# Kernel tuning notes

Measured on AMD Instinct MI355X. Metric: run time of the kernel, lower is better.

Reference implementation:

```python
import jax, jax.numpy as jnp
import numpy as np

N = 1048576   # samples
C = 64        # classes (Y unique targets)
S = 8         # subgroups


def setup_inputs() -> dict:
    key = jax.random.key(0)
    k1, k2, k3 = jax.random.split(key, 3)
    logits = jax.random.normal(k1, (N, C), dtype=jnp.float32)
    targets = jax.random.randint(k2, (N,), 0, C, dtype=jnp.int64)
    subgroup_inf = jax.random.randint(k3, (N,), 0, S, dtype=jnp.int64)
    return {"logits": logits, "targets": targets, "subgroup_inf": subgroup_inf}


def reference(logits, targets, subgroup_inf):
    # per-sample cross-entropy (loss_fn with reduction='none')
    logp = jax.nn.log_softmax(logits, axis=-1)                       # [N, C]
    per_sample = -jnp.take_along_axis(logp, targets[:, None], axis=-1)[:, 0]  # [N]

    # composite (target, subgroup) key -> group counts via one scatter-add
    key_ids = targets * S + subgroup_inf                              # [N]
    counts = jax.ops.segment_sum(jnp.ones_like(per_sample), key_ids,
                                 num_segments=C * S)                  # [C*S]
    # every sample's own group has count >= 1, so no div-by-zero
    weighted = per_sample / counts[key_ids]
    return jnp.sum(weighted)
```

## Files before the change

### kernel.cpp

```cpp
#include <hip/hip_runtime.h>


#define NKEYS 512
typedef float v4f __attribute__((ext_vector_type(4)));

__device__ __forceinline__ float pick4(v4f v, int j) {
    float r = v.x;
    r = (j == 1) ? v.y : r;
    r = (j == 2) ? v.z : r;
    r = (j == 3) ? v.w : r;
    return r;
}

__device__ __forceinline__ float esum4(v4f v) {
    return __expf(v.x) + __expf(v.y) + __expf(v.z) + __expf(v.w);
}

__global__ __launch_bounds__(256)
void orl_fused_kernel(const float* __restrict__ logits,
                      const int* __restrict__ targets,
                      const int* __restrict__ subg,
                      float* __restrict__ gsum,
                      unsigned int* __restrict__ gcnt,
                      int n) {
    __shared__ float        lsum[NKEYS];
    __shared__ unsigned int lcnt[NKEYS];
    for (int i = threadIdx.x; i < NKEYS; i += 256) { lsum[i] = 0.0f; lcnt[i] = 0u; }
    __syncthreads();

    const int lane = threadIdx.x & 63;
    const int q    = lane & 15;
    const int g    = lane >> 4;
    const int wave = (blockIdx.x << 2) | (threadIdx.x >> 6);
    const int nwaves = gridDim.x << 2;

    int base = wave * 16;
    for (; base + 16 <= n; base += nwaves * 16) {
        const int r0 = base + g, r1 = base + 4 + g, r2 = base + 8 + g, r3 = base + 12 + g;
        const v4f v0 = __builtin_nontemporal_load((const v4f*)(logits + (size_t)r0 * 64) + q);
        const v4f v1 = __builtin_nontemporal_load((const v4f*)(logits + (size_t)r1 * 64) + q);
        const v4f v2 = __builtin_nontemporal_load((const v4f*)(logits + (size_t)r2 * 64) + q);
        const v4f v3 = __builtin_nontemporal_load((const v4f*)(logits + (size_t)r3 * 64) + q);
        const int t0 = targets[r0], t1 = targets[r1], t2 = targets[r2], t3 = targets[r3];

        float s0 = esum4(v0), s1 = esum4(v1), s2 = esum4(v2), s3 = esum4(v3);
        #pragma unroll
        for (int m = 1; m < 16; m <<= 1) {
            s0 += __shfl_xor(s0, m, 16);
            s1 += __shfl_xor(s1, m, 16);
            s2 += __shfl_xor(s2, m, 16);
            s3 += __shfl_xor(s3, m, 16);
        }
        if ((t0 >> 2) == q) {
            const float ps = __logf(s0) - pick4(v0, t0 & 3);
            const int key = t0 * 8 + subg[r0];
            atomicAdd(&lsum[key], ps); atomicAdd(&lcnt[key], 1u);
        }
        if ((t1 >> 2) == q) {
            const float ps = __logf(s1) - pick4(v1, t1 & 3);
            const int key = t1 * 8 + subg[r1];
            atomicAdd(&lsum[key], ps); atomicAdd(&lcnt[key], 1u);
        }
        if ((t2 >> 2) == q) {
            const float ps = __logf(s2) - pick4(v2, t2 & 3);
            const int key = t2 * 8 + subg[r2];
            atomicAdd(&lsum[key], ps); atomicAdd(&lcnt[key], 1u);
        }
        if ((t3 >> 2) == q) {
            const float ps = __logf(s3) - pick4(v3, t3 & 3);
            const int key = t3 * 8 + subg[r3];
            atomicAdd(&lsum[key], ps); atomicAdd(&lcnt[key], 1u);
        }
    }
    for (int o = 0; o < 16; o += 4) {
        const int r = base + o + g;
        if (r < n) {
            const v4f v = *((const v4f*)(logits + (size_t)r * 64) + q);
            const int t = targets[r];
            float s = esum4(v);
            #pragma unroll
            for (int m = 1; m < 16; m <<= 1) s += __shfl_xor(s, m, 16);
            if ((t >> 2) == q) {
                const float ps = __logf(s) - pick4(v, t & 3);
                const int key = t * 8 + subg[r];
                atomicAdd(&lsum[key], ps); atomicAdd(&lcnt[key], 1u);
            }
        }
    }

    __syncthreads();
    for (int i = threadIdx.x; i < NKEYS; i += 256) {
        const unsigned int c = lcnt[i];
        if (c) {
            atomicAdd(&gsum[i], lsum[i]);
            atomicAdd(&gcnt[i], c);
        }
    }
}

__global__ __launch_bounds__(512)
void orl_final_kernel(const float* __restrict__ gsum,
                      const unsigned int* __restrict__ gcnt,
                      float* __restrict__ out) {
    const int k = threadIdx.x;
    const unsigned int c = gcnt[k];
    float v = c ? gsum[k] / (float)c : 0.0f;
    #pragma unroll
    for (int m = 32; m > 0; m >>= 1) v += __shfl_down(v, m, 64);
    __shared__ float wsum[8];
    if ((k & 63) == 0) wsum[k >> 6] = v;
    __syncthreads();
    if (k == 0) {
        float t = 0.0f;
        #pragma unroll
        for (int w = 0; w < 8; ++w) t += wsum[w];
        out[0] = t;
    }
}

extern "C" void kernel_launch(void* const* d_in, const int* in_sizes, int n_in,
                              void* d_out, int out_size, void* d_ws, size_t ws_size,
                              hipStream_t stream) {
    const float* logits  = (const float*)d_in[0];
    const int*   targets = (const int*)d_in[1];
    const int*   subg    = (const int*)d_in[2];
    const int n = in_sizes[1];
    float* out = (float*)d_out;

    float*        gsum = (float*)d_ws;
    unsigned int* gcnt = (unsigned int*)((char*)d_ws + NKEYS * sizeof(float));

    hipMemsetAsync(d_ws, 0, NKEYS * (sizeof(float) + sizeof(unsigned int)), stream);

    orl_fused_kernel<<<2048, 256, 0, stream>>>(logits, targets, subg, gsum, gcnt, n);
    orl_final_kernel<<<1, 512, 0, stream>>>(gsum, gcnt, out);
}
```

Before: 385.5 us.

## Replace global atomics and memset with per-block partial histograms and a reduce pass

Each block now writes its full 512-key shared histogram to its own slice in workspace, and a single 1024-thread block reduces all slices. This drops the memset and the global atomic adds. The grid shrinks from 2048 to 512 blocks, so each wave handles more rows. Subgroup loads are also hoisted so they are issued alongside the target loads. In exchange, the reduce kernel now reads 2 MB of partials serially from one block, and the smaller grid may hide memory latency less well.

```diff
diff --git a/kernel.cpp b/kernel.cpp
--- a/kernel.cpp
+++ b/kernel.cpp
@@ -2,6 +2,7 @@
 
 
 #define NKEYS 512
+#define NSLICES 512
 typedef float v4f __attribute__((ext_vector_type(4)));
 
 __device__ __forceinline__ float pick4(v4f v, int j) {
@@ -17,12 +18,12 @@
 }
 
 __global__ __launch_bounds__(256)
-void orl_fused_kernel(const float* __restrict__ logits,
-                      const int* __restrict__ targets,
-                      const int* __restrict__ subg,
-                      float* __restrict__ gsum,
-                      unsigned int* __restrict__ gcnt,
-                      int n) {
+void orl_hist_kernel(const float* __restrict__ logits,
+                     const int* __restrict__ targets,
+                     const int* __restrict__ subg,
+                     float* __restrict__ psum,
+                     unsigned int* __restrict__ pcnt,
+                     int n) {
     __shared__ float        lsum[NKEYS];
     __shared__ unsigned int lcnt[NKEYS];
     for (int i = threadIdx.x; i < NKEYS; i += 256) { lsum[i] = 0.0f; lcnt[i] = 0u; }
@@ -42,6 +43,7 @@
         const v4f v2 = __builtin_nontemporal_load((const v4f*)(logits + (size_t)r2 * 64) + q);
         const v4f v3 = __builtin_nontemporal_load((const v4f*)(logits + (size_t)r3 * 64) + q);
         const int t0 = targets[r0], t1 = targets[r1], t2 = targets[r2], t3 = targets[r3];
+        const int u0 = subg[r0],    u1 = subg[r1],    u2 = subg[r2],    u3 = subg[r3];
 
         float s0 = esum4(v0), s1 = esum4(v1), s2 = esum4(v2), s3 = esum4(v3);
         #pragma unroll
@@ -53,23 +55,19 @@
         }
         if ((t0 >> 2) == q) {
             const float ps = __logf(s0) - pick4(v0, t0 & 3);
-            const int key = t0 * 8 + subg[r0];
-            atomicAdd(&lsum[key], ps); atomicAdd(&lcnt[key], 1u);
+            atomicAdd(&lsum[t0 * 8 + u0], ps); atomicAdd(&lcnt[t0 * 8 + u0], 1u);
         }
         if ((t1 >> 2) == q) {
             const float ps = __logf(s1) - pick4(v1, t1 & 3);
-            const int key = t1 * 8 + subg[r1];
-            atomicAdd(&lsum[key], ps); atomicAdd(&lcnt[key], 1u);
+            atomicAdd(&lsum[t1 * 8 + u1], ps); atomicAdd(&lcnt[t1 * 8 + u1], 1u);
         }
         if ((t2 >> 2) == q) {
             const float ps = __logf(s2) - pick4(v2, t2 & 3);
-            const int key = t2 * 8 + subg[r2];
-            atomicAdd(&lsum[key], ps); atomicAdd(&lcnt[key], 1u);
+            atomicAdd(&lsum[t2 * 8 + u2], ps); atomicAdd(&lcnt[t2 * 8 + u2], 1u);
         }
         if ((t3 >> 2) == q) {
             const float ps = __logf(s3) - pick4(v3, t3 & 3);
-            const int key = t3 * 8 + subg[r3];
-            atomicAdd(&lsum[key], ps); atomicAdd(&lcnt[key], 1u);
+            atomicAdd(&lsum[t3 * 8 + u3], ps); atomicAdd(&lcnt[t3 * 8 + u3], 1u);
         }
     }
     for (int o = 0; o < 16; o += 4) {
@@ -89,32 +87,47 @@
     }
 
     __syncthreads();
+    const size_t sbase = (size_t)blockIdx.x * NKEYS;
     for (int i = threadIdx.x; i < NKEYS; i += 256) {
-        const unsigned int c = lcnt[i];
-        if (c) {
-            atomicAdd(&gsum[i], lsum[i]);
-            atomicAdd(&gcnt[i], c);
-        }
+        psum[sbase + i] = lsum[i];
+        pcnt[sbase + i] = lcnt[i];
     }
 }
 
-__global__ __launch_bounds__(512)
-void orl_final_kernel(const float* __restrict__ gsum,
-                      const unsigned int* __restrict__ gcnt,
-                      float* __restrict__ out) {
-    const int k = threadIdx.x;
-    const unsigned int c = gcnt[k];
-    float v = c ? gsum[k] / (float)c : 0.0f;
+__global__ __launch_bounds__(1024)
+void orl_reduce_kernel(const float* __restrict__ psum,
+                       const unsigned int* __restrict__ pcnt,
+                       float* __restrict__ out) {
+    const int t = threadIdx.x;
+    const int k = t & (NKEYS - 1);
+    const int h = t >> 9;
+    float s = 0.0f; unsigned int c = 0u;
+    const int b0 = h * (NSLICES / 2);
+    #pragma unroll 8
+    for (int b = b0; b < b0 + NSLICES / 2; ++b) {
+        s += psum[(size_t)b * NKEYS + k];
+        c += pcnt[(size_t)b * NKEYS + k];
+    }
+    __shared__ float        s2[NKEYS];
+    __shared__ unsigned int c2[NKEYS];
+    if (h) { s2[k] = s; c2[k] = c; }
+    __syncthreads();
+    float v = 0.0f;
+    if (!h) {
+        const float S = s + s2[k];
+        const unsigned int C = c + c2[k];
+        v = C ? S / (float)C : 0.0f;
+    }
     #pragma unroll
     for (int m = 32; m > 0; m >>= 1) v += __shfl_down(v, m, 64);
-    __shared__ float wsum[8];
-    if ((k & 63) == 0) wsum[k >> 6] = v;
+    __shared__ float wred[16];
+    if ((t & 63) == 0) wred[t >> 6] = v;
     __syncthreads();
-    if (k == 0) {
-        float t = 0.0f;
+    if (t == 0) {
+        float r = 0.0f;
         #pragma unroll
-        for (int w = 0; w < 8; ++w) t += wsum[w];
-        out[0] = t;
+        for (int w = 0; w < 16; ++w) r += wred[w];
+        out[0] = r;
     }
 }
 
@@ -127,11 +140,9 @@
     const int n = in_sizes[1];
     float* out = (float*)d_out;
 
-    float*        gsum = (float*)d_ws;
-    unsigned int* gcnt = (unsigned int*)((char*)d_ws + NKEYS * sizeof(float));
+    float*        psum = (float*)d_ws;
+    unsigned int* pcnt = (unsigned int*)((char*)d_ws + (size_t)NSLICES * NKEYS * 4);
 
-    hipMemsetAsync(d_ws, 0, NKEYS * (sizeof(float) + sizeof(unsigned int)), stream);
-
-    orl_fused_kernel<<<2048, 256, 0, stream>>>(logits, targets, subg, gsum, gcnt, n);
-    orl_final_kernel<<<1, 512, 0, stream>>>(gsum, gcnt, out);
+    orl_hist_kernel<<<NSLICES, 256, 0, stream>>>(logits, targets, subg, psum, pcnt, n);
+    orl_reduce_kernel<<<1, 1024, 0, stream>>>(psum, pcnt, out);
 }
```

Measured after the change: 373.2 us. 1.03x faster.
